# Kernel tuning notes

Measured on AMD Instinct MI355X. Metric: run time of the kernel, lower is better.

The kernel has to match this reference:

```python
import jax, jax.numpy as jnp
import numpy as np

EPS = 1e-05


def setup_inputs() -> dict:
    key = jax.random.key(0)
    x = jax.random.normal(key, (256, 256, 256), dtype=jnp.float32)
    return {"x": x}


def reference(x):
    # x: [B, N, N] dependency score logits
    B, N, _ = x.shape
    eye = jnp.eye(N, dtype=x.dtype)
    exp_x = jnp.exp(x)                                  # [B, N, N]
    diag_exp = jnp.exp(jnp.diagonal(x, axis1=-2, axis2=-1))  # [B, N] root scores

    # Build Laplacian: zero diagonal, negate off-diagonals, column sums on diag
    lap = (exp_x + EPS) * (1.0 - eye)                   # masked_fill diag with 0
    colsum = lap.sum(axis=-2)                           # torch sum(0) = column sums
    lap = -lap + colsum[:, None, :] * eye               # -lap + diag(colsum)
    # Replace row 0 with exp of the diagonal of input (root selection row)
    lap = lap.at[:, 0, :].set(diag_exp)

    inv = jnp.linalg.inv(lap)                           # batched inverse [B, N, N]
    d = jnp.diagonal(inv, axis1=-2, axis2=-1)           # [B, N]

    term1 = exp_x * d[:, None, :]                       # factor[i,j] = inv_diag[j]
    term2 = exp_x * jnp.swapaxes(inv, -1, -2)
    term1 = term1.at[:, :, 0].set(0.0)
    term2 = term2.at[:, 0, :].set(0.0)
    out = term1 - term2

    roots = diag_exp * inv[:, :, 0]                     # inv.T[0] == inv[:, 0]
    out = out + eye * roots[:, :, None]                 # add diag(roots)
    return out
```

## Files before the change

### kernel.cpp

```cpp
#include <hip/hip_runtime.h>
#include <math.h>

#define N 256
#define BS 32
#define NB_ 8
#define EPS 1e-5f

__global__ __launch_bounds__(512, 2) void mtt_fused(const float* __restrict__ x,
                                                    float* __restrict__ out) {
    constexpr int LDR = N + 8;
    __shared__ alignas(16) float  Rf[BS][LDR];
    __shared__ alignas(16) float  CfT[BS][LDR];
    __shared__ double Ps[BS][BS + 1];
    __shared__ float  Pf[BS][BS + 1];
    __shared__ double dsum[2][N];
    __shared__ float  sdx[N];
    __shared__ float  sdiag_f[N];
    __shared__ float  sroot_f[N];
    __shared__ int    indx[BS];

    const int tid = threadIdx.x;
    const int ty = tid >> 5, tx = tid & 31;
    const int R0  = ty << 4;
    const int c0a = tx << 2;
    const int c0b = 128 + (tx << 2);
    const float* xb = x + (size_t)blockIdx.x * N * N;
    float* ob = out + (size_t)blockIdx.x * N * N;

    float m[16][8];

    double csacc = 0.0;
    const int tq = tid >> 8, jc = tid & 255;
#pragma unroll 1
    for (int s = 0; s < 8; ++s) {
        {
            const int rl = tid >> 4, cl = (tid & 15) << 4;
            const float* src = &xb[(size_t)(32 * s + rl) * N + cl];
            *(float4*)&Rf[rl][cl]      = *(const float4*)&src[0];
            *(float4*)&Rf[rl][cl + 4]  = *(const float4*)&src[4];
            *(float4*)&Rf[rl][cl + 8]  = *(const float4*)&src[8];
            *(float4*)&Rf[rl][cl + 12] = *(const float4*)&src[12];
        }
        __syncthreads();
#pragma unroll
        for (int r = 0; r < 16; ++r)
            csacc += (double)expf(Rf[(tq << 4) + r][jc]);
        if (tid < 32) sdx[32 * s + tid] = expf(Rf[tid][32 * s + tid]);
        if ((tx >> 3) == s) {
            const int jb = (tx & 7) << 2;
#pragma unroll
            for (int cc = 0; cc < 4; ++cc)
#pragma unroll
                for (int r = 0; r < 16; ++r)
                    m[r][cc] = -(expf(Rf[jb + cc][R0 + r]) + EPS);
        }
        if (s >= 4 && (tx >> 3) == s - 4) {
            const int jb = (tx & 7) << 2;
#pragma unroll
            for (int cc = 0; cc < 4; ++cc)
#pragma unroll
                for (int r = 0; r < 16; ++r)
                    m[r][4 + cc] = -(expf(Rf[jb + cc][R0 + r]) + EPS);
        }
        __syncthreads();
    }
    dsum[tq][jc] = csacc;
    __syncthreads();
    if (tid < N) dsum[0][tid] += dsum[1][tid];
    __syncthreads();
    if (ty < 8) {
#pragma unroll
        for (int r = 0; r < 16; ++r) {
            const int i = R0 + r;
            if (tx == (i >> 2) && i != 0)
                m[r][r & 3] =
                    (float)(dsum[0][i] - (double)sdx[i] + 255.0 * (double)EPS);
        }
    } else {
#pragma unroll
        for (int r = 0; r < 16; ++r) {
            const int i = R0 + r;
            if (tx == ((i - 128) >> 2))
                m[r][4 + (r & 3)] =
                    (float)(dsum[0][i] - (double)sdx[i] + 255.0 * (double)EPS);
        }
    }
    if (tx == 0) {
#pragma unroll
        for (int r = 0; r < 16; ++r) m[r][0] = sdx[R0 + r];
    }

#pragma unroll 1
    for (int kb = 0; kb < NB_; ++kb) {
        const bool rowOwner = (ty >> 1) == kb;
        const bool h0piv = (kb < 4) && ((tx >> 3) == kb);
        const bool h1piv = (kb >= 4) && ((tx >> 3) == kb - 4);
        const int lr = (ty - (kb << 1)) << 4;
        const int lc = (tx & 7) << 2;

        if (rowOwner) {
#pragma unroll
            for (int r = 0; r < 16; ++r) {
                *(float4*)&Rf[lr + r][c0a] =
                    make_float4(m[r][0], m[r][1], m[r][2], m[r][3]);
                *(float4*)&Rf[lr + r][c0b] =
                    make_float4(m[r][4], m[r][5], m[r][6], m[r][7]);
            }
        }
        if (h0piv) {
#pragma unroll
            for (int cc = 0; cc < 4; ++cc) {
                *(float4*)&CfT[lc + cc][R0]      = make_float4(m[0][cc],  m[1][cc],  m[2][cc],  m[3][cc]);
                *(float4*)&CfT[lc + cc][R0 + 4]  = make_float4(m[4][cc],  m[5][cc],  m[6][cc],  m[7][cc]);
                *(float4*)&CfT[lc + cc][R0 + 8]  = make_float4(m[8][cc],  m[9][cc],  m[10][cc], m[11][cc]);
                *(float4*)&CfT[lc + cc][R0 + 12] = make_float4(m[12][cc], m[13][cc], m[14][cc], m[15][cc]);
            }
            if (rowOwner) {
#pragma unroll
                for (int r = 0; r < 16; ++r)
#pragma unroll
                    for (int cc = 0; cc < 4; ++cc)
                        Ps[lr + r][lc + cc] = (double)m[r][cc];
            }
        }
        if (h1piv) {
#pragma unroll
            for (int cc = 0; cc < 4; ++cc) {
                *(float4*)&CfT[lc + cc][R0]      = make_float4(m[0][4+cc],  m[1][4+cc],  m[2][4+cc],  m[3][4+cc]);
                *(float4*)&CfT[lc + cc][R0 + 4]  = make_float4(m[4][4+cc],  m[5][4+cc],  m[6][4+cc],  m[7][4+cc]);
                *(float4*)&CfT[lc + cc][R0 + 8]  = make_float4(m[8][4+cc],  m[9][4+cc],  m[10][4+cc], m[11][4+cc]);
                *(float4*)&CfT[lc + cc][R0 + 12] = make_float4(m[12][4+cc], m[13][4+cc], m[14][4+cc], m[15][4+cc]);
            }
            if (rowOwner) {
#pragma unroll
                for (int r = 0; r < 16; ++r)
#pragma unroll
                    for (int cc = 0; cc < 4; ++cc)
                        Ps[lr + r][lc + cc] = (double)m[r][4 + cc];
            }
        }
        __syncthreads();

        {
            const int rr = tid & 31;
            const int r0 = ty, r1 = ty + 16, c = tx;
#pragma unroll 1
            for (int k2 = 0; k2 < BS; ++k2) {
                double v  = Ps[rr][k2];
                double av = (rr >= k2) ? fabs(v) : -1.0;
                int idx = rr;
#pragma unroll
                for (int off = 1; off < 64; off <<= 1) {
                    const double oav = __shfl_xor(av, off);
                    const double ov  = __shfl_xor(v, off);
                    const int    oi  = __shfl_xor(idx, off);
                    if (oav > av || (oav == av && oi < idx)) { av = oav; v = ov; idx = oi; }
                }
                const int p = idx;
                const double pivinv = 1.0 / v;
                if (tid == 0) indx[k2] = p;
                const int sr0 = (r0 == k2) ? p : ((r0 == p) ? k2 : r0);
                const int sr1 = (r1 == k2) ? p : ((r1 == p) ? k2 : r1);
                const double prow  = Ps[p][c];
                const double aval0 = Ps[sr0][c], scol0 = Ps[sr0][k2];
                const double aval1 = Ps[sr1][c], scol1 = Ps[sr1][k2];
                __syncthreads();
                const double srw = (c == k2) ? pivinv : prow * pivinv;
                const double b0  = (c == k2) ? 0.0 : aval0;
                const double b1  = (c == k2) ? 0.0 : aval1;
                Ps[r0][c] = (r0 == k2) ? srw : fma(-scol0, srw, b0);
                Ps[r1][c] = (r1 == k2) ? srw : fma(-scol1, srw, b1);
                __syncthreads();
            }
            if (tid < 32) {
                for (int k2 = BS - 1; k2 >= 0; --k2) {
                    const int p = indx[k2];
                    if (p != k2) {
                        double t = Ps[tid][k2];
                        Ps[tid][k2] = Ps[tid][p];
                        Ps[tid][p]  = t;
                    }
                }
            }
            __syncthreads();
            Pf[ty][tx]      = (float)Ps[ty][tx];
            Pf[ty + 16][tx] = (float)Ps[ty + 16][tx];
            __syncthreads();
        }

        {
            float a0[8], a1[8];
#pragma unroll
            for (int c = 0; c < 8; ++c) { a0[c] = 0.f; a1[c] = 0.f; }
#pragma unroll 2
            for (int mm = 0; mm < BS; ++mm) {
                const float p0 = Pf[ty][mm];
                const float p1 = Pf[ty + 16][mm];
                const float4 r0 = *(const float4*)&Rf[mm][c0a];
                const float4 r1 = *(const float4*)&Rf[mm][c0b];
                a0[0] = fmaf(p0, r0.x, a0[0]);  a1[0] = fmaf(p1, r0.x, a1[0]);
                a0[1] = fmaf(p0, r0.y, a0[1]);  a1[1] = fmaf(p1, r0.y, a1[1]);
                a0[2] = fmaf(p0, r0.z, a0[2]);  a1[2] = fmaf(p1, r0.z, a1[2]);
                a0[3] = fmaf(p0, r0.w, a0[3]);  a1[3] = fmaf(p1, r0.w, a1[3]);
                a0[4] = fmaf(p0, r1.x, a0[4]);  a1[4] = fmaf(p1, r1.x, a1[4]);
                a0[5] = fmaf(p0, r1.y, a0[5]);  a1[5] = fmaf(p1, r1.y, a1[5]);
                a0[6] = fmaf(p0, r1.z, a0[6]);  a1[6] = fmaf(p1, r1.z, a1[6]);
                a0[7] = fmaf(p0, r1.w, a0[7]);  a1[7] = fmaf(p1, r1.w, a1[7]);
            }
            if (h0piv) {
#pragma unroll
                for (int cc = 0; cc < 4; ++cc) {
                    a0[cc] = Pf[ty][lc + cc];
                    a1[cc] = Pf[ty + 16][lc + cc];
                }
            }
            if (h1piv) {
#pragma unroll
                for (int cc = 0; cc < 4; ++cc) {
                    a0[4 + cc] = Pf[ty][lc + cc];
                    a1[4 + cc] = Pf[ty + 16][lc + cc];
                }
            }
            __syncthreads();
            *(float4*)&Rf[ty][c0a]      = make_float4(a0[0], a0[1], a0[2], a0[3]);
            *(float4*)&Rf[ty][c0b]      = make_float4(a0[4], a0[5], a0[6], a0[7]);
            *(float4*)&Rf[ty + 16][c0a] = make_float4(a1[0], a1[1], a1[2], a1[3]);
            *(float4*)&Rf[ty + 16][c0b] = make_float4(a1[4], a1[5], a1[6], a1[7]);
        }
        __syncthreads();

        if (rowOwner) {
#pragma unroll
            for (int r = 0; r < 16; ++r) {
                const float4 b0 = *(const float4*)&Rf[lr + r][c0a];
                const float4 b1 = *(const float4*)&Rf[lr + r][c0b];
                m[r][0] = b0.x; m[r][1] = b0.y; m[r][2] = b0.z; m[r][3] = b0.w;
                m[r][4] = b1.x; m[r][5] = b1.y; m[r][6] = b1.z; m[r][7] = b1.w;
            }
        } else {
            if (h0piv) {
#pragma unroll
                for (int r = 0; r < 16; ++r) {
                    m[r][0] = 0.f; m[r][1] = 0.f; m[r][2] = 0.f; m[r][3] = 0.f;
                }
            }
            if (h1piv) {
#pragma unroll
                for (int r = 0; r < 16; ++r) {
                    m[r][4] = 0.f; m[r][5] = 0.f; m[r][6] = 0.f; m[r][7] = 0.f;
                }
            }
#pragma unroll 2
            for (int mm = 0; mm < BS; ++mm) {
                const float4 rv0 = *(const float4*)&Rf[mm][c0a];
                const float4 rv1 = *(const float4*)&Rf[mm][c0b];
                const float4 cv0 = *(const float4*)&CfT[mm][R0];
                const float4 cv1 = *(const float4*)&CfT[mm][R0 + 4];
                const float4 cv2 = *(const float4*)&CfT[mm][R0 + 8];
                const float4 cv3 = *(const float4*)&CfT[mm][R0 + 12];
                const float cc16[16] = {cv0.x, cv0.y, cv0.z, cv0.w,
                                        cv1.x, cv1.y, cv1.z, cv1.w,
                                        cv2.x, cv2.y, cv2.z, cv2.w,
                                        cv3.x, cv3.y, cv3.z, cv3.w};
#pragma unroll
                for (int r = 0; r < 16; ++r) {
                    const float cr = -cc16[r];
                    m[r][0] = fmaf(cr, rv0.x, m[r][0]);
                    m[r][1] = fmaf(cr, rv0.y, m[r][1]);
                    m[r][2] = fmaf(cr, rv0.z, m[r][2]);
                    m[r][3] = fmaf(cr, rv0.w, m[r][3]);
                    m[r][4] = fmaf(cr, rv1.x, m[r][4]);
                    m[r][5] = fmaf(cr, rv1.y, m[r][5]);
                    m[r][6] = fmaf(cr, rv1.z, m[r][6]);
                    m[r][7] = fmaf(cr, rv1.w, m[r][7]);
                }
            }
        }
        __syncthreads();
    }

    if (ty < 8) {
#pragma unroll
        for (int r = 0; r < 16; ++r) {
            const int i = R0 + r;
            if (tx == (i >> 2)) sdiag_f[i] = m[r][r & 3];
        }
    } else {
#pragma unroll
        for (int r = 0; r < 16; ++r) {
            const int i = R0 + r;
            if (tx == ((i - 128) >> 2)) sdiag_f[i] = m[r][4 + (r & 3)];
        }
    }
    if (ty == 0) {
        *(float4*)&sroot_f[c0a] = make_float4(m[0][0], m[0][1], m[0][2], m[0][3]);
        *(float4*)&sroot_f[c0b] = make_float4(m[0][4], m[0][5], m[0][6], m[0][7]);
    }
    __syncthreads();

    float sd[8];
    {
        const float4 s0 = *(const float4*)&sdiag_f[c0a];
        const float4 s1 = *(const float4*)&sdiag_f[c0b];
        sd[0] = s0.x; sd[1] = s0.y; sd[2] = s0.z; sd[3] = s0.w;
        sd[4] = s1.x; sd[5] = s1.y; sd[6] = s1.z; sd[7] = s1.w;
    }
#pragma unroll
    for (int r = 0; r < 16; ++r) {
        const int a = R0 + r;
        const float4 x0 = *(const float4*)&xb[(size_t)a * N + c0a];
        const float4 x1 = *(const float4*)&xb[(size_t)a * N + c0b];
        const float xv[8] = {x0.x, x0.y, x0.z, x0.w, x1.x, x1.y, x1.z, x1.w};
        const float rt = sroot_f[a];
        float ov[8];
#pragma unroll
        for (int c = 0; c < 8; ++c) {
            const int b_ = (c < 4) ? (c0a + c) : (c0b + (c - 4));
            const float e = expf(xv[c]);
            float o = (b_ == 0) ? 0.0f : e * sd[c];
            if (a != 0) o -= e * m[r][c];
            if (a == b_) o += e * rt;
            ov[c] = o;
        }
        *(float4*)&ob[(size_t)a * N + c0a] = make_float4(ov[0], ov[1], ov[2], ov[3]);
        *(float4*)&ob[(size_t)a * N + c0b] = make_float4(ov[4], ov[5], ov[6], ov[7]);
    }
}

extern "C" void kernel_launch(void* const* d_in, const int* in_sizes, int n_in,
                              void* d_out, int out_size, void* d_ws, size_t ws_size,
                              hipStream_t stream) {
    const float* x = (const float*)d_in[0];
    float* out = (float*)d_out;
    mtt_fused<<<256, 512, 0, stream>>>(x, out);
}
```

Measured before the change: 438.3 us.

## Double block size to 1024 threads, halving per-thread register tile to 8x8

Each block now uses 1024 threads instead of 512, so every thread holds an 8x8 register tile of the 256x256 matrix rather than 16x8. The partial column-sum reduction, the panel inversion (one row per thread) and the trailing update are re-indexed to match. The goal is more waves per block to hide latency on the serial pivot loop, with fewer registers per thread. In exchange each barrier now synchronises twice as many waves, and the launch bound of 1024 with 4 blocks may be unachievable given the shared-memory footprint.

```diff
diff --git a/kernel.cpp b/kernel.cpp
--- a/kernel.cpp
+++ b/kernel.cpp
@@ -6,14 +6,14 @@
 #define NB_ 8
 #define EPS 1e-5f
 
-__global__ __launch_bounds__(512, 2) void mtt_fused(const float* __restrict__ x,
-                                                    float* __restrict__ out) {
+__global__ __launch_bounds__(1024, 4) void mtt_fused(const float* __restrict__ x,
+                                                     float* __restrict__ out) {
     constexpr int LDR = N + 8;
     __shared__ alignas(16) float  Rf[BS][LDR];
     __shared__ alignas(16) float  CfT[BS][LDR];
     __shared__ double Ps[BS][BS + 1];
     __shared__ float  Pf[BS][BS + 1];
-    __shared__ double dsum[2][N];
+    __shared__ double dsum[4][N];
     __shared__ float  sdx[N];
     __shared__ float  sdiag_f[N];
     __shared__ float  sroot_f[N];
@@ -21,37 +21,35 @@
 
     const int tid = threadIdx.x;
     const int ty = tid >> 5, tx = tid & 31;
-    const int R0  = ty << 4;
+    const int R0  = ty << 3;
     const int c0a = tx << 2;
     const int c0b = 128 + (tx << 2);
     const float* xb = x + (size_t)blockIdx.x * N * N;
     float* ob = out + (size_t)blockIdx.x * N * N;
 
-    float m[16][8];
+    float m[8][8];
 
     double csacc = 0.0;
     const int tq = tid >> 8, jc = tid & 255;
 #pragma unroll 1
     for (int s = 0; s < 8; ++s) {
         {
-            const int rl = tid >> 4, cl = (tid & 15) << 4;
+            const int rl = tid >> 5, cl = (tid & 31) << 3;
             const float* src = &xb[(size_t)(32 * s + rl) * N + cl];
-            *(float4*)&Rf[rl][cl]      = *(const float4*)&src[0];
-            *(float4*)&Rf[rl][cl + 4]  = *(const float4*)&src[4];
-            *(float4*)&Rf[rl][cl + 8]  = *(const float4*)&src[8];
-            *(float4*)&Rf[rl][cl + 12] = *(const float4*)&src[12];
-        }
-        __syncthreads();
-#pragma unroll
-        for (int r = 0; r < 16; ++r)
-            csacc += (double)expf(Rf[(tq << 4) + r][jc]);
+            *(float4*)&Rf[rl][cl]     = *(const float4*)&src[0];
+            *(float4*)&Rf[rl][cl + 4] = *(const float4*)&src[4];
+        }
+        __syncthreads();
+#pragma unroll
+        for (int r = 0; r < 8; ++r)
+            csacc += (double)expf(Rf[(tq << 3) + r][jc]);
         if (tid < 32) sdx[32 * s + tid] = expf(Rf[tid][32 * s + tid]);
         if ((tx >> 3) == s) {
             const int jb = (tx & 7) << 2;
 #pragma unroll
             for (int cc = 0; cc < 4; ++cc)
 #pragma unroll
-                for (int r = 0; r < 16; ++r)
+                for (int r = 0; r < 8; ++r)
                     m[r][cc] = -(expf(Rf[jb + cc][R0 + r]) + EPS);
         }
         if (s >= 4 && (tx >> 3) == s - 4) {
@@ -59,48 +57,49 @@
 #pragma unroll
             for (int cc = 0; cc < 4; ++cc)
 #pragma unroll
-                for (int r = 0; r < 16; ++r)
+                for (int r = 0; r < 8; ++r)
                     m[r][4 + cc] = -(expf(Rf[jb + cc][R0 + r]) + EPS);
         }
         __syncthreads();
     }
     dsum[tq][jc] = csacc;
     __syncthreads();
-    if (tid < N) dsum[0][tid] += dsum[1][tid];
+    if (tid < N)
+        dsum[0][tid] = dsum[0][tid] + dsum[1][tid] + dsum[2][tid] + dsum[3][tid];
     __syncthreads();
-    if (ty < 8) {
-#pragma unroll
-        for (int r = 0; r < 16; ++r) {
+    if (ty < 16) {
+#pragma unroll
+        for (int r = 0; r < 8; ++r) {
             const int i = R0 + r;
-            if (tx == (i >> 2) && i != 0)
+            if (tx == ((ty << 1) + (r >> 2)) && i != 0)
                 m[r][r & 3] =
                     (float)(dsum[0][i] - (double)sdx[i] + 255.0 * (double)EPS);
         }
     } else {
 #pragma unroll
-        for (int r = 0; r < 16; ++r) {
+        for (int r = 0; r < 8; ++r) {
             const int i = R0 + r;
-            if (tx == ((i - 128) >> 2))
+            if (tx == (((ty - 16) << 1) + (r >> 2)))
                 m[r][4 + (r & 3)] =
                     (float)(dsum[0][i] - (double)sdx[i] + 255.0 * (double)EPS);
         }
     }
     if (tx == 0) {
 #pragma unroll
-        for (int r = 0; r < 16; ++r) m[r][0] = sdx[R0 + r];
+        for (int r = 0; r < 8; ++r) m[r][0] = sdx[R0 + r];
     }
 
 #pragma unroll 1
     for (int kb = 0; kb < NB_; ++kb) {
-        const bool rowOwner = (ty >> 1) == kb;
+        const bool rowOwner = (ty >> 2) == kb;
         const bool h0piv = (kb < 4) && ((tx >> 3) == kb);
         const bool h1piv = (kb >= 4) && ((tx >> 3) == kb - 4);
-        const int lr = (ty - (kb << 1)) << 4;
+        const int lr = (ty & 3) << 3;
         const int lc = (tx & 7) << 2;
 
         if (rowOwner) {
 #pragma unroll
-            for (int r = 0; r < 16; ++r) {
+            for (int r = 0; r < 8; ++r) {
                 *(float4*)&Rf[lr + r][c0a] =
                     make_float4(m[r][0], m[r][1], m[r][2], m[r][3]);
                 *(float4*)&Rf[lr + r][c0b] =
@@ -110,14 +109,14 @@
         if (h0piv) {
 #pragma unroll
             for (int cc = 0; cc < 4; ++cc) {
-                *(float4*)&CfT[lc + cc][R0]      = make_float4(m[0][cc],  m[1][cc],  m[2][cc],  m[3][cc]);
-                *(float4*)&CfT[lc + cc][R0 + 4]  = make_float4(m[4][cc],  m[5][cc],  m[6][cc],  m[7][cc]);
-                *(float4*)&CfT[lc + cc][R0 + 8]  = make_float4(m[8][cc],  m[9][cc],  m[10][cc], m[11][cc]);
-                *(float4*)&CfT[lc + cc][R0 + 12] = make_float4(m[12][cc], m[13][cc], m[14][cc], m[15][cc]);
+                *(float4*)&CfT[lc + cc][R0] =
+                    make_float4(m[0][cc], m[1][cc], m[2][cc], m[3][cc]);
+                *(float4*)&CfT[lc + cc][R0 + 4] =
+                    make_float4(m[4][cc], m[5][cc], m[6][cc], m[7][cc]);
             }
             if (rowOwner) {
 #pragma unroll
-                for (int r = 0; r < 16; ++r)
+                for (int r = 0; r < 8; ++r)
 #pragma unroll
                     for (int cc = 0; cc < 4; ++cc)
                         Ps[lr + r][lc + cc] = (double)m[r][cc];
@@ -126,14 +125,14 @@
         if (h1piv) {
 #pragma unroll
             for (int cc = 0; cc < 4; ++cc) {
-                *(float4*)&CfT[lc + cc][R0]      = make_float4(m[0][4+cc],  m[1][4+cc],  m[2][4+cc],  m[3][4+cc]);
-                *(float4*)&CfT[lc + cc][R0 + 4]  = make_float4(m[4][4+cc],  m[5][4+cc],  m[6][4+cc],  m[7][4+cc]);
-                *(float4*)&CfT[lc + cc][R0 + 8]  = make_float4(m[8][4+cc],  m[9][4+cc],  m[10][4+cc], m[11][4+cc]);
-                *(float4*)&CfT[lc + cc][R0 + 12] = make_float4(m[12][4+cc], m[13][4+cc], m[14][4+cc], m[15][4+cc]);
+                *(float4*)&CfT[lc + cc][R0] =
+                    make_float4(m[0][4 + cc], m[1][4 + cc], m[2][4 + cc], m[3][4 + cc]);
+                *(float4*)&CfT[lc + cc][R0 + 4] =
+                    make_float4(m[4][4 + cc], m[5][4 + cc], m[6][4 + cc], m[7][4 + cc]);
             }
             if (rowOwner) {
 #pragma unroll
-                for (int r = 0; r < 16; ++r)
+                for (int r = 0; r < 8; ++r)
 #pragma unroll
                     for (int cc = 0; cc < 4; ++cc)
                         Ps[lr + r][lc + cc] = (double)m[r][4 + cc];
@@ -143,7 +142,7 @@
 
         {
             const int rr = tid & 31;
-            const int r0 = ty, r1 = ty + 16, c = tx;
+            const int r = ty, c = tx;
 #pragma unroll 1
             for (int k2 = 0; k2 < BS; ++k2) {
                 double v  = Ps[rr][k2];
@@ -159,17 +158,13 @@
                 const int p = idx;
                 const double pivinv = 1.0 / v;
                 if (tid == 0) indx[k2] = p;
-                const int sr0 = (r0 == k2) ? p : ((r0 == p) ? k2 : r0);
-                const int sr1 = (r1 == k2) ? p : ((r1 == p) ? k2 : r1);
-                const double prow  = Ps[p][c];
-                const double aval0 = Ps[sr0][c], scol0 = Ps[sr0][k2];
-                const double aval1 = Ps[sr1][c], scol1 = Ps[sr1][k2];
+                const int sr = (r == k2) ? p : ((r == p) ? k2 : r);
+                const double prow = Ps[p][c];
+                const double aval = Ps[sr][c], scol = Ps[sr][k2];
                 __syncthreads();
                 const double srw = (c == k2) ? pivinv : prow * pivinv;
-                const double b0  = (c == k2) ? 0.0 : aval0;
-                const double b1  = (c == k2) ? 0.0 : aval1;
-                Ps[r0][c] = (r0 == k2) ? srw : fma(-scol0, srw, b0);
-                Ps[r1][c] = (r1 == k2) ? srw : fma(-scol1, srw, b1);
+                const double base = (c == k2) ? 0.0 : aval;
+                Ps[r][c] = (r == k2) ? srw : fma(-scol, srw, base);
                 __syncthreads();
             }
             if (tid < 32) {
@@ -183,55 +178,45 @@
                 }
             }
             __syncthreads();
-            Pf[ty][tx]      = (float)Ps[ty][tx];
-            Pf[ty + 16][tx] = (float)Ps[ty + 16][tx];
+            Pf[ty][tx] = (float)Ps[ty][tx];
             __syncthreads();
         }
 
         {
-            float a0[8], a1[8];
-#pragma unroll
-            for (int c = 0; c < 8; ++c) { a0[c] = 0.f; a1[c] = 0.f; }
+            float a0[8];
+#pragma unroll
+            for (int c = 0; c < 8; ++c) a0[c] = 0.f;
 #pragma unroll 2
             for (int mm = 0; mm < BS; ++mm) {
                 const float p0 = Pf[ty][mm];
-                const float p1 = Pf[ty + 16][mm];
                 const float4 r0 = *(const float4*)&Rf[mm][c0a];
                 const float4 r1 = *(const float4*)&Rf[mm][c0b];
-                a0[0] = fmaf(p0, r0.x, a0[0]);  a1[0] = fmaf(p1, r0.x, a1[0]);
-                a0[1] = fmaf(p0, r0.y, a0[1]);  a1[1] = fmaf(p1, r0.y, a1[1]);
-                a0[2] = fmaf(p0, r0.z, a0[2]);  a1[2] = fmaf(p1, r0.z, a1[2]);
-                a0[3] = fmaf(p0, r0.w, a0[3]);  a1[3] = fmaf(p1, r0.w, a1[3]);
-                a0[4] = fmaf(p0, r1.x, a0[4]);  a1[4] = fmaf(p1, r1.x, a1[4]);
-                a0[5] = fmaf(p0, r1.y, a0[5]);  a1[5] = fmaf(p1, r1.y, a1[5]);
-                a0[6] = fmaf(p0, r1.z, a0[6]);  a1[6] = fmaf(p1, r1.z, a1[6]);
-                a0[7] = fmaf(p0, r1.w, a0[7]);  a1[7] = fmaf(p1, r1.w, a1[7]);
+                a0[0] = fmaf(p0, r0.x, a0[0]);
+                a0[1] = fmaf(p0, r0.y, a0[1]);
+                a0[2] = fmaf(p0, r0.z, a0[2]);
+                a0[3] = fmaf(p0, r0.w, a0[3]);
+                a0[4] = fmaf(p0, r1.x, a0[4]);
+                a0[5] = fmaf(p0, r1.y, a0[5]);
+                a0[6] = fmaf(p0, r1.z, a0[6]);
+                a0[7] = fmaf(p0, r1.w, a0[7]);
             }
             if (h0piv) {
 #pragma unroll
-                for (int cc = 0; cc < 4; ++cc) {
-                    a0[cc] = Pf[ty][lc + cc];
-                    a1[cc] = Pf[ty + 16][lc + cc];
-                }
+                for (int cc = 0; cc < 4; ++cc) a0[cc] = Pf[ty][lc + cc];
             }
             if (h1piv) {
 #pragma unroll
-                for (int cc = 0; cc < 4; ++cc) {
-                    a0[4 + cc] = Pf[ty][lc + cc];
-                    a1[4 + cc] = Pf[ty + 16][lc + cc];
-                }
+                for (int cc = 0; cc < 4; ++cc) a0[4 + cc] = Pf[ty][lc + cc];
             }
             __syncthreads();
-            *(float4*)&Rf[ty][c0a]      = make_float4(a0[0], a0[1], a0[2], a0[3]);
-            *(float4*)&Rf[ty][c0b]      = make_float4(a0[4], a0[5], a0[6], a0[7]);
-            *(float4*)&Rf[ty + 16][c0a] = make_float4(a1[0], a1[1], a1[2], a1[3]);
-            *(float4*)&Rf[ty + 16][c0b] = make_float4(a1[4], a1[5], a1[6], a1[7]);
+            *(float4*)&Rf[ty][c0a] = make_float4(a0[0], a0[1], a0[2], a0[3]);
+            *(float4*)&Rf[ty][c0b] = make_float4(a0[4], a0[5], a0[6], a0[7]);
         }
         __syncthreads();
 
         if (rowOwner) {
 #pragma unroll
-            for (int r = 0; r < 16; ++r) {
+            for (int r = 0; r < 8; ++r) {
                 const float4 b0 = *(const float4*)&Rf[lr + r][c0a];
                 const float4 b1 = *(const float4*)&Rf[lr + r][c0b];
                 m[r][0] = b0.x; m[r][1] = b0.y; m[r][2] = b0.z; m[r][3] = b0.w;
@@ -240,13 +225,13 @@
         } else {
             if (h0piv) {
 #pragma unroll
-                for (int r = 0; r < 16; ++r) {
+                for (int r = 0; r < 8; ++r) {
                     m[r][0] = 0.f; m[r][1] = 0.f; m[r][2] = 0.f; m[r][3] = 0.f;
                 }
             }
             if (h1piv) {
 #pragma unroll
-                for (int r = 0; r < 16; ++r) {
+                for (int r = 0; r < 8; ++r) {
                     m[r][4] = 0.f; m[r][5] = 0.f; m[r][6] = 0.f; m[r][7] = 0.f;
                 }
             }
@@ -256,40 +241,78 @@
                 const float4 rv1 = *(const float4*)&Rf[mm][c0b];
                 const float4 cv0 = *(const float4*)&CfT[mm][R0];
                 const float4 cv1 = *(const float4*)&CfT[mm][R0 + 4];
-                const float4 cv2 = *(const float4*)&CfT[mm][R0 + 8];
-                const float4 cv3 = *(const float4*)&CfT[mm][R0 + 12];
-                const float cc16[16] = {cv0.x, cv0.y, cv0.z, cv0.w,
-                                        cv1.x, cv1.y, cv1.z, cv1.w,
-                                        cv2.x, cv2.y, cv2.z, cv2.w,
-                                        cv3.x, cv3.y, cv3.z, cv3.w};
-#pragma unroll
-                for (int r = 0; r < 16; ++r) {
-                    const float cr = -cc16[r];
-                    m[r][0] = fmaf(cr, rv0.x, m[r][0]);
-                    m[r][1] = fmaf(cr, rv0.y, m[r][1]);
-                    m[r][2] = fmaf(cr, rv0.z, m[r][2]);
-                    m[r][3] = fmaf(cr, rv0.w, m[r][3]);
-                    m[r][4] = fmaf(cr, rv1.x, m[r][4]);
-                    m[r][5] = fmaf(cr, rv1.y, m[r][5]);
-                    m[r][6] = fmaf(cr, rv1.z, m[r][6]);
-                    m[r][7] = fmaf(cr, rv1.w, m[r][7]);
-                }
-            }
-        }
-        __syncthreads();
-    }
-
-    if (ty < 8) {
-#pragma unroll
-        for (int r = 0; r < 16; ++r) {
+                {
+                    const float cr = -cv0.x;
+                    m[0][0] = fmaf(cr, rv0.x, m[0][0]); m[0][1] = fmaf(cr, rv0.y, m[0][1]);
+                    m[0][2] = fmaf(cr, rv0.z, m[0][2]); m[0][3] = fmaf(cr, rv0.w, m[0][3]);
+                    m[0][4] = fmaf(cr, rv1.x, m[0][4]); m[0][5] = fmaf(cr, rv1.y, m[0][5]);
+                    m[0][6] = fmaf(cr, rv1.z, m[0][6]); m[0][7] = fmaf(cr, rv1.w, m[0][7]);
+                }
+                {
+                    const float cr = -cv0.y;
+                    m[1][0] = fmaf(cr, rv0.x, m[1][0]); m[1][1] = fmaf(cr, rv0.y, m[1][1]);
+                    m[1][2] = fmaf(cr, rv0.z, m[1][2]); m[1][3] = fmaf(cr, rv0.w, m[1][3]);
+                    m[1][4] = fmaf(cr, rv1.x, m[1][4]); m[1][5] = fmaf(cr, rv1.y, m[1][5]);
+                    m[1][6] = fmaf(cr, rv1.z, m[1][6]); m[1][7] = fmaf(cr, rv1.w, m[1][7]);
+                }
+                {
+                    const float cr = -cv0.z;
+                    m[2][0] = fmaf(cr, rv0.x, m[2][0]); m[2][1] = fmaf(cr, rv0.y, m[2][1]);
+                    m[2][2] = fmaf(cr, rv0.z, m[2][2]); m[2][3] = fmaf(cr, rv0.w, m[2][3]);
+                    m[2][4] = fmaf(cr, rv1.x, m[2][4]); m[2][5] = fmaf(cr, rv1.y, m[2][5]);
+                    m[2][6] = fmaf(cr, rv1.z, m[2][6]); m[2][7] = fmaf(cr, rv1.w, m[2][7]);
+                }
+                {
+                    const float cr = -cv0.w;
+                    m[3][0] = fmaf(cr, rv0.x, m[3][0]); m[3][1] = fmaf(cr, rv0.y, m[3][1]);
+                    m[3][2] = fmaf(cr, rv0.z, m[3][2]); m[3][3] = fmaf(cr, rv0.w, m[3][3]);
+                    m[3][4] = fmaf(cr, rv1.x, m[3][4]); m[3][5] = fmaf(cr, rv1.y, m[3][5]);
+                    m[3][6] = fmaf(cr, rv1.z, m[3][6]); m[3][7] = fmaf(cr, rv1.w, m[3][7]);
+                }
+                {
+                    const float cr = -cv1.x;
+                    m[4][0] = fmaf(cr, rv0.x, m[4][0]); m[4][1] = fmaf(cr, rv0.y, m[4][1]);
+                    m[4][2] = fmaf(cr, rv0.z, m[4][2]); m[4][3] = fmaf(cr, rv0.w, m[4][3]);
+                    m[4][4] = fmaf(cr, rv1.x, m[4][4]); m[4][5] = fmaf(cr, rv1.y, m[4][5]);
+                    m[4][6] = fmaf(cr, rv1.z, m[4][6]); m[4][7] = fmaf(cr, rv1.w, m[4][7]);
+                }
+                {
+                    const float cr = -cv1.y;
+                    m[5][0] = fmaf(cr, rv0.x, m[5][0]); m[5][1] = fmaf(cr, rv0.y, m[5][1]);
+                    m[5][2] = fmaf(cr, rv0.z, m[5][2]); m[5][3] = fmaf(cr, rv0.w, m[5][3]);
+                    m[5][4] = fmaf(cr, rv1.x, m[5][4]); m[5][5] = fmaf(cr, rv1.y, m[5][5]);
+                    m[5][6] = fmaf(cr, rv1.z, m[5][6]); m[5][7] = fmaf(cr, rv1.w, m[5][7]);
+                }
+                {
+                    const float cr = -cv1.z;
+                    m[6][0] = fmaf(cr, rv0.x, m[6][0]); m[6][1] = fmaf(cr, rv0.y, m[6][1]);
+                    m[6][2] = fmaf(cr, rv0.z, m[6][2]); m[6][3] = fmaf(cr, rv0.w, m[6][3]);
+                    m[6][4] = fmaf(cr, rv1.x, m[6][4]); m[6][5] = fmaf(cr, rv1.y, m[6][5]);
+                    m[6][6] = fmaf(cr, rv1.z, m[6][6]); m[6][7] = fmaf(cr, rv1.w, m[6][7]);
+                }
+                {
+                    const float cr = -cv1.w;
+                    m[7][0] = fmaf(cr, rv0.x, m[7][0]); m[7][1] = fmaf(cr, rv0.y, m[7][1]);
+                    m[7][2] = fmaf(cr, rv0.z, m[7][2]); m[7][3] = fmaf(cr, rv0.w, m[7][3]);
+                    m[7][4] = fmaf(cr, rv1.x, m[7][4]); m[7][5] = fmaf(cr, rv1.y, m[7][5]);
+                    m[7][6] = fmaf(cr, rv1.z, m[7][6]); m[7][7] = fmaf(cr, rv1.w, m[7][7]);
+                }
+            }
+        }
+        __syncthreads();
+    }
+
+    if (ty < 16) {
+#pragma unroll
+        for (int r = 0; r < 8; ++r) {
             const int i = R0 + r;
-            if (tx == (i >> 2)) sdiag_f[i] = m[r][r & 3];
+            if (tx == ((ty << 1) + (r >> 2))) sdiag_f[i] = m[r][r & 3];
         }
     } else {
 #pragma unroll
-        for (int r = 0; r < 16; ++r) {
+        for (int r = 0; r < 8; ++r) {
             const int i = R0 + r;
-            if (tx == ((i - 128) >> 2)) sdiag_f[i] = m[r][4 + (r & 3)];
+            if (tx == (((ty - 16) << 1) + (r >> 2))) sdiag_f[i] = m[r][4 + (r & 3)];
         }
     }
     if (ty == 0) {
@@ -306,7 +329,7 @@
         sd[4] = s1.x; sd[5] = s1.y; sd[6] = s1.z; sd[7] = s1.w;
     }
 #pragma unroll
-    for (int r = 0; r < 16; ++r) {
+    for (int r = 0; r < 8; ++r) {
         const int a = R0 + r;
         const float4 x0 = *(const float4*)&xb[(size_t)a * N + c0a];
         const float4 x1 = *(const float4*)&xb[(size_t)a * N + c0b];
@@ -332,5 +355,5 @@
                               hipStream_t stream) {
     const float* x = (const float*)d_in[0];
     float* out = (float*)d_out;
-    mtt_fused<<<256, 512, 0, stream>>>(x, out);
+    mtt_fused<<<256, 1024, 0, stream>>>(x, out);
 }
```

Result: slower. 633.5 us (+44.5%).

## Invert pivot block in registers within one wavefront, double-buffer row panel

Applied to the files above, without the earlier changes.

The 32x32 diagonal-block Gauss-Jordan inversion moves out of a shared double array updated by all 512 threads with two barriers per pivot step. It now runs in registers inside a single 64-lane wavefront, using shuffles for the pivot search, row swap and elimination. The row panel is split into two shared buffers, so the write-back of the updated panel no longer needs an extra barrier. This removes about 64 block-wide barriers per block step, at the cost of leaving the other waves idle during the inversion and adding register pressure from the 16 doubles per lane.

```diff
diff --git a/kernel.cpp b/kernel.cpp
--- a/kernel.cpp
+++ b/kernel.cpp
@@ -9,9 +9,9 @@
 __global__ __launch_bounds__(512, 2) void mtt_fused(const float* __restrict__ x,
                                                     float* __restrict__ out) {
     constexpr int LDR = N + 8;
-    __shared__ alignas(16) float  Rf[BS][LDR];
+    __shared__ alignas(16) float  RfA[BS][LDR];
+    __shared__ alignas(16) float  RfB[BS][LDR];
     __shared__ alignas(16) float  CfT[BS][LDR];
-    __shared__ double Ps[BS][BS + 1];
     __shared__ float  Pf[BS][BS + 1];
     __shared__ double dsum[2][N];
     __shared__ float  sdx[N];
@@ -36,23 +36,23 @@
         {
             const int rl = tid >> 4, cl = (tid & 15) << 4;
             const float* src = &xb[(size_t)(32 * s + rl) * N + cl];
-            *(float4*)&Rf[rl][cl]      = *(const float4*)&src[0];
-            *(float4*)&Rf[rl][cl + 4]  = *(const float4*)&src[4];
-            *(float4*)&Rf[rl][cl + 8]  = *(const float4*)&src[8];
-            *(float4*)&Rf[rl][cl + 12] = *(const float4*)&src[12];
+            *(float4*)&RfA[rl][cl]      = *(const float4*)&src[0];
+            *(float4*)&RfA[rl][cl + 4]  = *(const float4*)&src[4];
+            *(float4*)&RfA[rl][cl + 8]  = *(const float4*)&src[8];
+            *(float4*)&RfA[rl][cl + 12] = *(const float4*)&src[12];
         }
         __syncthreads();
 #pragma unroll
         for (int r = 0; r < 16; ++r)
-            csacc += (double)expf(Rf[(tq << 4) + r][jc]);
-        if (tid < 32) sdx[32 * s + tid] = expf(Rf[tid][32 * s + tid]);
+            csacc += (double)expf(RfA[(tq << 4) + r][jc]);
+        if (tid < 32) sdx[32 * s + tid] = expf(RfA[tid][32 * s + tid]);
         if ((tx >> 3) == s) {
             const int jb = (tx & 7) << 2;
 #pragma unroll
             for (int cc = 0; cc < 4; ++cc)
 #pragma unroll
                 for (int r = 0; r < 16; ++r)
-                    m[r][cc] = -(expf(Rf[jb + cc][R0 + r]) + EPS);
+                    m[r][cc] = -(expf(RfA[jb + cc][R0 + r]) + EPS);
         }
         if (s >= 4 && (tx >> 3) == s - 4) {
             const int jb = (tx & 7) << 2;
@@ -60,7 +60,7 @@
             for (int cc = 0; cc < 4; ++cc)
 #pragma unroll
                 for (int r = 0; r < 16; ++r)
-                    m[r][4 + cc] = -(expf(Rf[jb + cc][R0 + r]) + EPS);
+                    m[r][4 + cc] = -(expf(RfA[jb + cc][R0 + r]) + EPS);
         }
         __syncthreads();
     }
@@ -92,6 +92,7 @@
 
 #pragma unroll 1
     for (int kb = 0; kb < NB_; ++kb) {
+        const int k0 = kb * BS;
         const bool rowOwner = (ty >> 1) == kb;
         const bool h0piv = (kb < 4) && ((tx >> 3) == kb);
         const bool h1piv = (kb >= 4) && ((tx >> 3) == kb - 4);
@@ -101,9 +102,9 @@
         if (rowOwner) {
 #pragma unroll
             for (int r = 0; r < 16; ++r) {
-                *(float4*)&Rf[lr + r][c0a] =
+                *(float4*)&RfA[lr + r][c0a] =
                     make_float4(m[r][0], m[r][1], m[r][2], m[r][3]);
-                *(float4*)&Rf[lr + r][c0b] =
+                *(float4*)&RfA[lr + r][c0b] =
                     make_float4(m[r][4], m[r][5], m[r][6], m[r][7]);
             }
         }
@@ -115,13 +116,6 @@
                 *(float4*)&CfT[lc + cc][R0 + 8]  = make_float4(m[8][cc],  m[9][cc],  m[10][cc], m[11][cc]);
                 *(float4*)&CfT[lc + cc][R0 + 12] = make_float4(m[12][cc], m[13][cc], m[14][cc], m[15][cc]);
             }
-            if (rowOwner) {
-#pragma unroll
-                for (int r = 0; r < 16; ++r)
-#pragma unroll
-                    for (int cc = 0; cc < 4; ++cc)
-                        Ps[lr + r][lc + cc] = (double)m[r][cc];
-            }
         }
         if (h1piv) {
 #pragma unroll
@@ -131,62 +125,67 @@
                 *(float4*)&CfT[lc + cc][R0 + 8]  = make_float4(m[8][4+cc],  m[9][4+cc],  m[10][4+cc], m[11][4+cc]);
                 *(float4*)&CfT[lc + cc][R0 + 12] = make_float4(m[12][4+cc], m[13][4+cc], m[14][4+cc], m[15][4+cc]);
             }
-            if (rowOwner) {
-#pragma unroll
-                for (int r = 0; r < 16; ++r)
-#pragma unroll
-                    for (int cc = 0; cc < 4; ++cc)
-                        Ps[lr + r][lc + cc] = (double)m[r][4 + cc];
-            }
-        }
-        __syncthreads();
-
-        {
-            const int rr = tid & 31;
-            const int r0 = ty, r1 = ty + 16, c = tx;
-#pragma unroll 1
+        }
+        __syncthreads();
+
+        if (tid < 64) {
+            const int l = tid;
+            const int row = l & 31;
+            const int h = l >> 5;
+            const int hb = h << 5;
+            double p[16];
+#pragma unroll
+            for (int j = 0; j < 16; ++j)
+                p[j] = (double)CfT[(h << 4) + j][k0 + row];
+
+#pragma unroll
             for (int k2 = 0; k2 < BS; ++k2) {
-                double v  = Ps[rr][k2];
-                double av = (rr >= k2) ? fabs(v) : -1.0;
-                int idx = rr;
+                const int hk2 = k2 >> 4, jk2 = k2 & 15;
+                const double cand = p[jk2];
+                double av = (h == hk2 && row >= k2) ? fabs(cand) : -1.0;
+                double vv = cand;
+                int idx = row;
 #pragma unroll
                 for (int off = 1; off < 64; off <<= 1) {
                     const double oav = __shfl_xor(av, off);
-                    const double ov  = __shfl_xor(v, off);
+                    const double ovv = __shfl_xor(vv, off);
                     const int    oi  = __shfl_xor(idx, off);
-                    if (oav > av || (oav == av && oi < idx)) { av = oav; v = ov; idx = oi; }
-                }
-                const int p = idx;
-                const double pivinv = 1.0 / v;
-                if (tid == 0) indx[k2] = p;
-                const int sr0 = (r0 == k2) ? p : ((r0 == p) ? k2 : r0);
-                const int sr1 = (r1 == k2) ? p : ((r1 == p) ? k2 : r1);
-                const double prow  = Ps[p][c];
-                const double aval0 = Ps[sr0][c], scol0 = Ps[sr0][k2];
-                const double aval1 = Ps[sr1][c], scol1 = Ps[sr1][k2];
-                __syncthreads();
-                const double srw = (c == k2) ? pivinv : prow * pivinv;
-                const double b0  = (c == k2) ? 0.0 : aval0;
-                const double b1  = (c == k2) ? 0.0 : aval1;
-                Ps[r0][c] = (r0 == k2) ? srw : fma(-scol0, srw, b0);
-                Ps[r1][c] = (r1 == k2) ? srw : fma(-scol1, srw, b1);
-                __syncthreads();
-            }
-            if (tid < 32) {
+                    if (oav > av || (oav == av && oi < idx)) { av = oav; vv = ovv; idx = oi; }
+                }
+                const double pivinv = 1.0 / vv;
+                if (l == 0) indx[k2] = idx;
+                const int prt = (row == k2) ? idx : ((row == idx) ? k2 : row);
+                const int sl = prt + hb;
+#pragma unroll
+                for (int j = 0; j < 16; ++j) p[j] = __shfl(p[j], sl);
+                const double scol = __shfl(p[jk2], row + (hk2 << 5));
+                const int pl = k2 + hb;
+                const bool isPivRow = (row == k2);
+#pragma unroll
+                for (int j = 0; j < 16; ++j) {
+                    const double prow = __shfl(p[j], pl);
+                    const bool isK2col = (h == hk2) && (j == jk2);
+                    const double srw  = isK2col ? pivinv : prow * pivinv;
+                    const double base = isK2col ? 0.0 : p[j];
+                    p[j] = isPivRow ? srw : fma(-scol, srw, base);
+                }
+            }
+#pragma unroll
+            for (int j = 0; j < 16; ++j)
+                Pf[row][(h << 4) + j] = (float)p[j];
+            if (l < 32) {
+#pragma unroll 1
                 for (int k2 = BS - 1; k2 >= 0; --k2) {
-                    const int p = indx[k2];
-                    if (p != k2) {
-                        double t = Ps[tid][k2];
-                        Ps[tid][k2] = Ps[tid][p];
-                        Ps[tid][p]  = t;
+                    const int pp = indx[k2];
+                    if (pp != k2) {
+                        const float t = Pf[l][k2];
+                        Pf[l][k2] = Pf[l][pp];
+                        Pf[l][pp] = t;
                     }
                 }
             }
-            __syncthreads();
-            Pf[ty][tx]      = (float)Ps[ty][tx];
-            Pf[ty + 16][tx] = (float)Ps[ty + 16][tx];
-            __syncthreads();
-        }
+        }
+        __syncthreads();
 
         {
             float a0[8], a1[8];
@@ -196,8 +195,8 @@
             for (int mm = 0; mm < BS; ++mm) {
                 const float p0 = Pf[ty][mm];
                 const float p1 = Pf[ty + 16][mm];
-                const float4 r0 = *(const float4*)&Rf[mm][c0a];
-                const float4 r1 = *(const float4*)&Rf[mm][c0b];
+                const float4 r0 = *(const float4*)&RfA[mm][c0a];
+                const float4 r1 = *(const float4*)&RfA[mm][c0b];
                 a0[0] = fmaf(p0, r0.x, a0[0]);  a1[0] = fmaf(p1, r0.x, a1[0]);
                 a0[1] = fmaf(p0, r0.y, a0[1]);  a1[1] = fmaf(p1, r0.y, a1[1]);
                 a0[2] = fmaf(p0, r0.z, a0[2]);  a1[2] = fmaf(p1, r0.z, a1[2]);
@@ -221,19 +220,18 @@
                     a1[4 + cc] = Pf[ty + 16][lc + cc];
                 }
             }
-            __syncthreads();
-            *(float4*)&Rf[ty][c0a]      = make_float4(a0[0], a0[1], a0[2], a0[3]);
-            *(float4*)&Rf[ty][c0b]      = make_float4(a0[4], a0[5], a0[6], a0[7]);
-            *(float4*)&Rf[ty + 16][c0a] = make_float4(a1[0], a1[1], a1[2], a1[3]);
-            *(float4*)&Rf[ty + 16][c0b] = make_float4(a1[4], a1[5], a1[6], a1[7]);
+            *(float4*)&RfB[ty][c0a]      = make_float4(a0[0], a0[1], a0[2], a0[3]);
+            *(float4*)&RfB[ty][c0b]      = make_float4(a0[4], a0[5], a0[6], a0[7]);
+            *(float4*)&RfB[ty + 16][c0a] = make_float4(a1[0], a1[1], a1[2], a1[3]);
+            *(float4*)&RfB[ty + 16][c0b] = make_float4(a1[4], a1[5], a1[6], a1[7]);
         }
         __syncthreads();
 
         if (rowOwner) {
 #pragma unroll
             for (int r = 0; r < 16; ++r) {
-                const float4 b0 = *(const float4*)&Rf[lr + r][c0a];
-                const float4 b1 = *(const float4*)&Rf[lr + r][c0b];
+                const float4 b0 = *(const float4*)&RfB[lr + r][c0a];
+                const float4 b1 = *(const float4*)&RfB[lr + r][c0b];
                 m[r][0] = b0.x; m[r][1] = b0.y; m[r][2] = b0.z; m[r][3] = b0.w;
                 m[r][4] = b1.x; m[r][5] = b1.y; m[r][6] = b1.z; m[r][7] = b1.w;
             }
@@ -252,8 +250,8 @@
             }
 #pragma unroll 2
             for (int mm = 0; mm < BS; ++mm) {
-                const float4 rv0 = *(const float4*)&Rf[mm][c0a];
-                const float4 rv1 = *(const float4*)&Rf[mm][c0b];
+                const float4 rv0 = *(const float4*)&RfB[mm][c0a];
+                const float4 rv1 = *(const float4*)&RfB[mm][c0b];
                 const float4 cv0 = *(const float4*)&CfT[mm][R0];
                 const float4 cv1 = *(const float4*)&CfT[mm][R0 + 4];
                 const float4 cv2 = *(const float4*)&CfT[mm][R0 + 8];
```

New measurement: 443.5 us. No clear change (+1.2%).
